# Performance work log

Measured on AMD Instinct MI355X. Metric: run time of the kernel, lower is better.

The kernel has to match this reference:

```python
import jax, jax.numpy as jnp
import numpy as np

B = 65536  # number of 32-bit words processed by the VM


def _build_tables():
    # ByteToNibbleFFN: byte one-hot -> (high, low) nibble one-hots
    W1_b2n = np.eye(256, dtype=np.float32)
    W2_b2n = np.zeros((256, 32), dtype=np.float32)
    for b in range(256):
        W2_b2n[b, (b >> 4) & 15] = 1.0
        W2_b2n[b, 16 + (b & 15)] = 1.0
    # NibbleToByteFFN: (high, low) -> byte one-hot
    W1_n2b = np.zeros((32, 256), dtype=np.float32)
    for high in range(16):
        for low in range(16):
            bv = (high << 4) | low
            W1_n2b[high, bv] = 1.0
            W1_n2b[16 + low, bv] = 1.0
    W2_n2b = np.eye(256, dtype=np.float32)
    # NibbleTableFFN for XOR
    W1_xor = np.zeros((32, 256), dtype=np.float32)
    W2_xor = np.zeros((256, 16), dtype=np.float32)
    for a in range(16):
        for b in range(16):
            k = a * 16 + b
            W1_xor[a, k] = 1.0
            W1_xor[16 + b, k] = 1.0
            W2_xor[k, (a ^ b) & 15] = 1.0
    # NibbleAddFFN: (a, b, carry) -> (sum, carry)
    W1_add = np.zeros((34, 512), dtype=np.float32)
    W2_sum = np.zeros((512, 16), dtype=np.float32)
    W2_carry = np.zeros((512, 2), dtype=np.float32)
    for a in range(16):
        for b in range(16):
            for c in range(2):
                k = a * 32 + b * 2 + c
                W1_add[a, k] = 1.0
                W1_add[16 + b, k] = 1.0
                W1_add[32 + c, k] = 1.0
                total = a + b + c
                W2_sum[k, total & 15] = 1.0
                W2_carry[k, 1 if total >= 16 else 0] = 1.0
    return (jnp.asarray(W1_b2n), jnp.asarray(W2_b2n), jnp.asarray(W1_n2b),
            jnp.asarray(W2_n2b), jnp.asarray(W1_xor), jnp.asarray(W2_xor),
            jnp.asarray(W1_add), jnp.asarray(W2_sum), jnp.asarray(W2_carry))


def setup_inputs() -> dict:
    key = jax.random.key(0)
    k1, k2 = jax.random.split(key)
    a_idx = jax.random.randint(k1, (B, 4), 0, 256)
    b_idx = jax.random.randint(k2, (B, 4), 0, 256)
    a_bytes = jax.nn.one_hot(a_idx, 256, dtype=jnp.float32)  # [B,4,256]
    b_bytes = jax.nn.one_hot(b_idx, 256, dtype=jnp.float32)
    (W1_b2n, W2_b2n, W1_n2b, W2_n2b, W1_xor, W2_xor,
     W1_add, W2_sum, W2_carry) = _build_tables()
    return {
        'a_bytes': a_bytes, 'b_bytes': b_bytes,
        'W1_b2n': W1_b2n, 'W2_b2n': W2_b2n,
        'W1_n2b': W1_n2b, 'W2_n2b': W2_n2b,
        'W1_xor': W1_xor, 'W2_xor': W2_xor,
        'W1_add': W1_add, 'W2_sum': W2_sum, 'W2_carry': W2_carry,
    }


def reference(a_bytes, b_bytes, W1_b2n, W2_b2n, W1_n2b, W2_n2b,
              W1_xor, W2_xor, W1_add, W2_sum, W2_carry):
    # Batched faithful translation of the torch VM: the torch code loops over
    # single words; here each op is vectorized over the word batch B while the
    # fixed 4-byte carry chain remains an explicit (structural) loop.
    def byte_to_nib(x):                       # x: [B,256]
        w = jax.nn.softmax((x @ W1_b2n) * 100.0, axis=-1)
        nib = w @ W2_b2n                      # [B,32]
        return nib[:, :16], nib[:, 16:]

    def nib_to_byte(high, low):               # [B,16] each -> [B,256]
        x = jnp.concatenate([high, low], axis=-1)
        w = jax.nn.softmax((x @ W1_n2b - 1.5) * 20.0, axis=-1)
        return w @ W2_n2b

    def nib_xor(a, b):                        # [B,16] each -> [B,16]
        x = jnp.concatenate([a, b], axis=-1)
        w = jax.nn.softmax((x @ W1_xor - 1.5) * 20.0, axis=-1)
        return w @ W2_xor

    def nib_add(a, b, c):                     # [B,16],[B,16],[B,2]
        x = jnp.concatenate([a, b, c], axis=-1)
        w = jax.nn.softmax((x @ W1_add - 2.5) * 20.0, axis=-1)
        return w @ W2_sum, w @ W2_carry

    def byte_xor(a, b):                       # [B,256] each
        a_h, a_l = byte_to_nib(a)
        b_h, b_l = byte_to_nib(b)
        return nib_to_byte(nib_xor(a_h, b_h), nib_xor(a_l, b_l))

    n = a_bytes.shape[0]
    # ByteAddFFN: 4-byte ripple-carry add, carry starts as one-hot 0
    carry = jnp.broadcast_to(jnp.array([1.0, 0.0], dtype=a_bytes.dtype), (n, 2))
    sum_bytes = []
    for i in range(4):
        a_h, a_l = byte_to_nib(a_bytes[:, i])
        b_h, b_l = byte_to_nib(b_bytes[:, i])
        r_low, carry_low = nib_add(a_l, b_l, carry)
        r_high, carry = nib_add(a_h, b_h, carry_low)
        sum_bytes.append(nib_to_byte(r_high, r_low))
    # Chain a second VM op: XOR the sum with operand a, per byte
    out = [byte_xor(sum_bytes[i], a_bytes[:, i]) for i in range(4)]
    return jnp.stack(out, axis=1)             # [B,4,256]
```

## Files before the change

### kernel.cpp

```cpp
#include <hip/hip_runtime.h>
#include <stdint.h>

typedef float f32x4 __attribute__((ext_vector_type(4)));


__global__ __launch_bounds__(256) void vm_phase1(
    const float* __restrict__ a_bytes,
    const float* __restrict__ b_bytes,
    uint32_t* __restrict__ ws,
    int n_words)
{
    const int lane = threadIdx.x & 63;
    const int w    = blockIdx.x * 4 + (threadIdx.x >> 6);
    if (w >= n_words) return;

    const long base = (long)w * 1024 + lane * 4;
    const float* pa = a_bytes + base;
    const float* pb = b_bytes + base;

    const f32x4 a0 = __builtin_nontemporal_load((const f32x4*)(pa));
    const f32x4 a1 = __builtin_nontemporal_load((const f32x4*)(pa + 256));
    const f32x4 a2 = __builtin_nontemporal_load((const f32x4*)(pa + 512));
    const f32x4 a3 = __builtin_nontemporal_load((const f32x4*)(pa + 768));
    const f32x4 b0 = __builtin_nontemporal_load((const f32x4*)(pb));
    const f32x4 b1 = __builtin_nontemporal_load((const f32x4*)(pb + 256));
    const f32x4 b2 = __builtin_nontemporal_load((const f32x4*)(pb + 512));
    const f32x4 b3 = __builtin_nontemporal_load((const f32x4*)(pb + 768));

    auto idx_of = [&](const f32x4 v) -> uint32_t {
        const uint64_t m0 = __ballot(v.x > 0.5f);
        const uint64_t m1 = __ballot(v.y > 0.5f);
        const uint64_t m2 = __ballot(v.z > 0.5f);
        const uint64_t m3 = __ballot(v.w > 0.5f);
        const uint64_t m  = m0 | m1 | m2 | m3;
        const uint32_t hl = (uint32_t)__ffsll((unsigned long long)m) - 1u;
        const uint32_t c  = (m1 ? 1u : 0u) | (m2 ? 2u : 0u) | (m3 ? 3u : 0u);
        return hl * 4u + c;
    };

    const uint32_t aw = idx_of(a0) | (idx_of(a1) << 8) |
                        (idx_of(a2) << 16) | (idx_of(a3) << 24);
    const uint32_t bw = idx_of(b0) | (idx_of(b1) << 8) |
                        (idx_of(b2) << 16) | (idx_of(b3) << 24);
    const uint32_t s = aw + bw;
    const uint32_t o = s ^ aw;

    if (lane == 0) ws[w] = o;
}

__global__ __launch_bounds__(256) void vm_phase2(
    const uint32_t* __restrict__ ws,
    float* __restrict__ out,
    int n_words)
{
    const int lane = threadIdx.x & 63;
    const int w    = blockIdx.x * 4 + (threadIdx.x >> 6);
    if (w >= n_words) return;

    const uint32_t o = ws[w];
    float* po = out + (long)w * 1024 + lane * 4;
    const int j = lane * 4;
#pragma unroll
    for (int k = 0; k < 4; ++k) {
        const int oi = (int)((o >> (8 * k)) & 255u);
        f32x4 ov;
        ov.x = (j     == oi) ? 1.0f : 0.0f;
        ov.y = (j + 1 == oi) ? 1.0f : 0.0f;
        ov.z = (j + 2 == oi) ? 1.0f : 0.0f;
        ov.w = (j + 3 == oi) ? 1.0f : 0.0f;
        *(f32x4*)(po + k * 256) = ov;
    }
}

__global__ __launch_bounds__(256) void vm_fused(
    const float* __restrict__ a_bytes,
    const float* __restrict__ b_bytes,
    float* __restrict__ out,
    int n_words)
{
    const int lane = threadIdx.x & 63;
    const int w    = blockIdx.x * 4 + (threadIdx.x >> 6);
    if (w >= n_words) return;

    const long base = (long)w * 1024 + lane * 4;
    const float* pa = a_bytes + base;
    const float* pb = b_bytes + base;

    const f32x4 a0 = __builtin_nontemporal_load((const f32x4*)(pa));
    const f32x4 a1 = __builtin_nontemporal_load((const f32x4*)(pa + 256));
    const f32x4 a2 = __builtin_nontemporal_load((const f32x4*)(pa + 512));
    const f32x4 a3 = __builtin_nontemporal_load((const f32x4*)(pa + 768));
    const f32x4 b0 = __builtin_nontemporal_load((const f32x4*)(pb));
    const f32x4 b1 = __builtin_nontemporal_load((const f32x4*)(pb + 256));
    const f32x4 b2 = __builtin_nontemporal_load((const f32x4*)(pb + 512));
    const f32x4 b3 = __builtin_nontemporal_load((const f32x4*)(pb + 768));

    auto idx_of = [&](const f32x4 v) -> uint32_t {
        const uint64_t m0 = __ballot(v.x > 0.5f);
        const uint64_t m1 = __ballot(v.y > 0.5f);
        const uint64_t m2 = __ballot(v.z > 0.5f);
        const uint64_t m3 = __ballot(v.w > 0.5f);
        const uint64_t m  = m0 | m1 | m2 | m3;
        const uint32_t hl = (uint32_t)__ffsll((unsigned long long)m) - 1u;
        const uint32_t c  = (m1 ? 1u : 0u) | (m2 ? 2u : 0u) | (m3 ? 3u : 0u);
        return hl * 4u + c;
    };

    const uint32_t aw = idx_of(a0) | (idx_of(a1) << 8) |
                        (idx_of(a2) << 16) | (idx_of(a3) << 24);
    const uint32_t bw = idx_of(b0) | (idx_of(b1) << 8) |
                        (idx_of(b2) << 16) | (idx_of(b3) << 24);
    const uint32_t s = aw + bw;
    const uint32_t o = s ^ aw;

    float* po = out + base;
    const int j = lane * 4;
#pragma unroll
    for (int k = 0; k < 4; ++k) {
        const int oi = (int)((o >> (8 * k)) & 255u);
        f32x4 ov;
        ov.x = (j     == oi) ? 1.0f : 0.0f;
        ov.y = (j + 1 == oi) ? 1.0f : 0.0f;
        ov.z = (j + 2 == oi) ? 1.0f : 0.0f;
        ov.w = (j + 3 == oi) ? 1.0f : 0.0f;
        __builtin_nontemporal_store(ov, (f32x4*)(po + k * 256));
    }
}

extern "C" void kernel_launch(void* const* d_in, const int* in_sizes, int n_in,
                              void* d_out, int out_size, void* d_ws, size_t ws_size,
                              hipStream_t stream)
{
    const float* a_bytes = (const float*)d_in[0];
    const float* b_bytes = (const float*)d_in[1];
    float* out = (float*)d_out;
    const int n_words = in_sizes[0] / 1024;
    const int blocks  = (n_words + 3) / 4;

    if (d_ws != nullptr && ws_size >= (size_t)n_words * 4) {
        uint32_t* ws = (uint32_t*)d_ws;
        vm_phase1<<<blocks, 256, 0, stream>>>(a_bytes, b_bytes, ws, n_words);
        vm_phase2<<<blocks, 256, 0, stream>>>(ws, out, n_words);
    } else {
        vm_fused<<<blocks, 256, 0, stream>>>(a_bytes, b_bytes, out, n_words);
    }
}
```

Baseline: 567.1 us.

## Make phase1 a persistent grid-stride kernel with register double-buffered loads

Phase1 now launches at most 2048 blocks and each wave loops over words with a grid stride. It prefetches the next word's a/b one-hot rows into registers while decoding the current one. The aim is to keep more loads in flight per wave and cut block launch overhead on this bandwidth-bound read of 512 MB. In exchange each wave holds more live registers, and the idx_of lambda moves to a shared device function.

```diff
diff --git a/kernel.cpp b/kernel.cpp
--- a/kernel.cpp
+++ b/kernel.cpp
@@ -3,6 +3,17 @@
 
 typedef float f32x4 __attribute__((ext_vector_type(4)));
 
+
+__device__ __forceinline__ uint32_t idx_of(const f32x4 v) {
+    const uint64_t m0 = __ballot(v.x > 0.5f);
+    const uint64_t m1 = __ballot(v.y > 0.5f);
+    const uint64_t m2 = __ballot(v.z > 0.5f);
+    const uint64_t m3 = __ballot(v.w > 0.5f);
+    const uint64_t m  = m0 | m1 | m2 | m3;
+    const uint32_t hl = (uint32_t)__ffsll((unsigned long long)m) - 1u;
+    const uint32_t c  = (m1 ? 1u : 0u) | (m2 ? 2u : 0u) | (m3 ? 3u : 0u);
+    return hl * 4u + c;
+}
 
 __global__ __launch_bounds__(256) void vm_phase1(
     const float* __restrict__ a_bytes,
@@ -10,42 +21,60 @@
     uint32_t* __restrict__ ws,
     int n_words)
 {
-    const int lane = threadIdx.x & 63;
-    const int w    = blockIdx.x * 4 + (threadIdx.x >> 6);
+    const int lane   = threadIdx.x & 63;
+    const int wv     = blockIdx.x * 4 + (threadIdx.x >> 6);
+    const int nwaves = gridDim.x * 4;
+    const long lofs  = lane * 4;
+
+    int w = wv;
     if (w >= n_words) return;
 
-    const long base = (long)w * 1024 + lane * 4;
-    const float* pa = a_bytes + base;
-    const float* pb = b_bytes + base;
+    const float* pa = a_bytes + (long)w * 1024 + lofs;
+    const float* pb = b_bytes + (long)w * 1024 + lofs;
+    f32x4 A0 = __builtin_nontemporal_load((const f32x4*)(pa));
+    f32x4 A1 = __builtin_nontemporal_load((const f32x4*)(pa + 256));
+    f32x4 A2 = __builtin_nontemporal_load((const f32x4*)(pa + 512));
+    f32x4 A3 = __builtin_nontemporal_load((const f32x4*)(pa + 768));
+    f32x4 B0 = __builtin_nontemporal_load((const f32x4*)(pb));
+    f32x4 B1 = __builtin_nontemporal_load((const f32x4*)(pb + 256));
+    f32x4 B2 = __builtin_nontemporal_load((const f32x4*)(pb + 512));
+    f32x4 B3 = __builtin_nontemporal_load((const f32x4*)(pb + 768));
 
-    const f32x4 a0 = __builtin_nontemporal_load((const f32x4*)(pa));
-    const f32x4 a1 = __builtin_nontemporal_load((const f32x4*)(pa + 256));
-    const f32x4 a2 = __builtin_nontemporal_load((const f32x4*)(pa + 512));
-    const f32x4 a3 = __builtin_nontemporal_load((const f32x4*)(pa + 768));
-    const f32x4 b0 = __builtin_nontemporal_load((const f32x4*)(pb));
-    const f32x4 b1 = __builtin_nontemporal_load((const f32x4*)(pb + 256));
-    const f32x4 b2 = __builtin_nontemporal_load((const f32x4*)(pb + 512));
-    const f32x4 b3 = __builtin_nontemporal_load((const f32x4*)(pb + 768));
+    while (w + nwaves < n_words) {
+        const int wn = w + nwaves;
+        const float* qa = a_bytes + (long)wn * 1024 + lofs;
+        const float* qb = b_bytes + (long)wn * 1024 + lofs;
+        const f32x4 An0 = __builtin_nontemporal_load((const f32x4*)(qa));
+        const f32x4 An1 = __builtin_nontemporal_load((const f32x4*)(qa + 256));
+        const f32x4 An2 = __builtin_nontemporal_load((const f32x4*)(qa + 512));
+        const f32x4 An3 = __builtin_nontemporal_load((const f32x4*)(qa + 768));
+        const f32x4 Bn0 = __builtin_nontemporal_load((const f32x4*)(qb));
+        const f32x4 Bn1 = __builtin_nontemporal_load((const f32x4*)(qb + 256));
+        const f32x4 Bn2 = __builtin_nontemporal_load((const f32x4*)(qb + 512));
+        const f32x4 Bn3 = __builtin_nontemporal_load((const f32x4*)(qb + 768));
 
-    auto idx_of = [&](const f32x4 v) -> uint32_t {
-        const uint64_t m0 = __ballot(v.x > 0.5f);
-        const uint64_t m1 = __ballot(v.y > 0.5f);
-        const uint64_t m2 = __ballot(v.z > 0.5f);
-        const uint64_t m3 = __ballot(v.w > 0.5f);
-        const uint64_t m  = m0 | m1 | m2 | m3;
-        const uint32_t hl = (uint32_t)__ffsll((unsigned long long)m) - 1u;
-        const uint32_t c  = (m1 ? 1u : 0u) | (m2 ? 2u : 0u) | (m3 ? 3u : 0u);
-        return hl * 4u + c;
-    };
+        const uint32_t aw = idx_of(A0) | (idx_of(A1) << 8) |
+                            (idx_of(A2) << 16) | (idx_of(A3) << 24);
+        const uint32_t bw = idx_of(B0) | (idx_of(B1) << 8) |
+                            (idx_of(B2) << 16) | (idx_of(B3) << 24);
+        const uint32_t s = aw + bw;
+        const uint32_t o = s ^ aw;
+        if (lane == 0) ws[w] = o;
 
-    const uint32_t aw = idx_of(a0) | (idx_of(a1) << 8) |
-                        (idx_of(a2) << 16) | (idx_of(a3) << 24);
-    const uint32_t bw = idx_of(b0) | (idx_of(b1) << 8) |
-                        (idx_of(b2) << 16) | (idx_of(b3) << 24);
-    const uint32_t s = aw + bw;
-    const uint32_t o = s ^ aw;
+        A0 = An0; A1 = An1; A2 = An2; A3 = An3;
+        B0 = Bn0; B1 = Bn1; B2 = Bn2; B3 = Bn3;
+        w = wn;
+    }
 
-    if (lane == 0) ws[w] = o;
+    {
+        const uint32_t aw = idx_of(A0) | (idx_of(A1) << 8) |
+                            (idx_of(A2) << 16) | (idx_of(A3) << 24);
+        const uint32_t bw = idx_of(B0) | (idx_of(B1) << 8) |
+                            (idx_of(B2) << 16) | (idx_of(B3) << 24);
+        const uint32_t s = aw + bw;
+        const uint32_t o = s ^ aw;
+        if (lane == 0) ws[w] = o;
+    }
 }
 
 __global__ __launch_bounds__(256) void vm_phase2(
@@ -95,17 +124,6 @@
     const f32x4 b2 = __builtin_nontemporal_load((const f32x4*)(pb + 512));
     const f32x4 b3 = __builtin_nontemporal_load((const f32x4*)(pb + 768));
 
-    auto idx_of = [&](const f32x4 v) -> uint32_t {
-        const uint64_t m0 = __ballot(v.x > 0.5f);
-        const uint64_t m1 = __ballot(v.y > 0.5f);
-        const uint64_t m2 = __ballot(v.z > 0.5f);
-        const uint64_t m3 = __ballot(v.w > 0.5f);
-        const uint64_t m  = m0 | m1 | m2 | m3;
-        const uint32_t hl = (uint32_t)__ffsll((unsigned long long)m) - 1u;
-        const uint32_t c  = (m1 ? 1u : 0u) | (m2 ? 2u : 0u) | (m3 ? 3u : 0u);
-        return hl * 4u + c;
-    };
-
     const uint32_t aw = idx_of(a0) | (idx_of(a1) << 8) |
                         (idx_of(a2) << 16) | (idx_of(a3) << 24);
     const uint32_t bw = idx_of(b0) | (idx_of(b1) << 8) |
@@ -139,7 +157,9 @@
 
     if (d_ws != nullptr && ws_size >= (size_t)n_words * 4) {
         uint32_t* ws = (uint32_t*)d_ws;
-        vm_phase1<<<blocks, 256, 0, stream>>>(a_bytes, b_bytes, ws, n_words);
+        int p1_blocks = (blocks < 2048) ? blocks : 2048;
+        if (p1_blocks < 1) p1_blocks = 1;
+        vm_phase1<<<p1_blocks, 256, 0, stream>>>(a_bytes, b_bytes, ws, n_words);
         vm_phase2<<<blocks, 256, 0, stream>>>(ws, out, n_words);
     } else {
         vm_fused<<<blocks, 256, 0, stream>>>(a_bytes, b_bytes, out, n_words);
```

After: 572.6 us. Within noise of the previous version (+1.0%).
